# Kernel tuning notes

Hardware: AMD Instinct MI355X
Metric: run time of the kernel (lower is better)

Reference implementation:

```python
import jax, jax.numpy as jnp
import numpy as np
from jax import lax

B, C, H, W = 32, 256, 56, 56
NH, LC, DIL = 8, 7, 8  # heads, window size, dilation; H == LC*DIL -> exact dilated partition
N = LC * LC
DH = C // NH
SCALE = DH ** (-0.5)


def _rel_index():
    ch = np.arange(LC)
    coords = np.stack(np.meshgrid(ch, ch, indexing='ij')).reshape(2, -1)  # (2, 49)
    rel = (coords[:, :, None] - coords[:, None, :]).transpose(1, 2, 0)  # (49,49,2)
    rel[..., 0] += LC - 1
    rel[..., 1] += LC - 1
    rel[..., 0] *= 2 * LC - 1
    return jnp.asarray(rel.sum(-1))  # (49,49) int

REL_IDX = _rel_index()


def _layernorm(x, w, b, eps=1e-5):
    m = x.mean(-1, keepdims=True)
    v = ((x - m) ** 2).mean(-1, keepdims=True)
    return (x - m) * lax.rsqrt(v + eps) * w + b


def setup_inputs() -> dict:
    key = jax.random.key(0)
    ks = jax.random.split(key, 8)
    def n(k, shape, s=0.02):
        return jax.random.normal(k, shape, jnp.float32) * s
    return {
        'x': jax.random.normal(ks[0], (B, C, H, W), jnp.float32),
        'cpe_w': n(ks[1], (C, 1, 3, 3)),
        'cpe_b': jnp.zeros((C,), jnp.float32),
        'ln1_w': jnp.ones((C,), jnp.float32),
        'ln1_b': jnp.zeros((C,), jnp.float32),
        'rpb': n(ks[2], ((2 * LC - 1) ** 2, NH)),
        'qkv_w': n(ks[3], (C, 3 * C)),
        'qkv_b': jnp.zeros((3 * C,), jnp.float32),
        'proj_w': n(ks[4], (C, C)),
        'proj_b': jnp.zeros((C,), jnp.float32),
        'ln2_w': jnp.ones((C,), jnp.float32),
        'ln2_b': jnp.zeros((C,), jnp.float32),
        'fc1_w': n(ks[5], (C, 4 * C)),
        'fc1_b': jnp.zeros((4 * C,), jnp.float32),
        'fc2_w': n(ks[6], (4 * C, C)),
        'fc2_b': jnp.zeros((C,), jnp.float32),
    }


def reference(x, cpe_w, cpe_b, ln1_w, ln1_b, rpb, qkv_w, qkv_b, proj_w, proj_b,
              ln2_w, ln2_b, fc1_w, fc1_b, fc2_w, fc2_b):
    # CPE: depthwise 3x3 conv, residual
    cpe = lax.conv_general_dilated(x, cpe_w, (1, 1), 'SAME',
                                   dimension_numbers=('NCHW', 'OIHW', 'NCHW'),
                                   feature_group_count=C)
    x = x + cpe + cpe_b[None, :, None, None]
    x = x.transpose(0, 2, 3, 1)  # B,H,W,C
    shortcut = x
    xn = _layernorm(x, ln1_w, ln1_b)
    # dilated window partition (LD!=0): window (i,j) gathers pixels (i+DIL*t, j+DIL*u)
    xw = xn.reshape(B, LC, DIL, LC, DIL, C).transpose(0, 2, 4, 1, 3, 5)  # B,i,j,t,u,C
    x1 = xw.reshape(B * DIL * DIL, N, C)
    # window attention with relative position bias
    qkv = (x1 @ qkv_w + qkv_b).reshape(-1, N, 3, NH, DH).transpose(2, 0, 3, 1, 4)
    q, k, v = qkv[0] * SCALE, qkv[1], qkv[2]  # (Bn,NH,N,DH)
    attn = jnp.einsum('bhnd,bhmd->bhnm', q, k)
    bias = rpb[REL_IDX].transpose(2, 0, 1)  # (NH,N,N)
    attn = jax.nn.softmax(attn + bias[None], axis=-1)
    o = jnp.einsum('bhnm,bhmd->bhnd', attn, v).transpose(0, 2, 1, 3).reshape(-1, N, C)
    o = o @ proj_w + proj_b
    # scatter windows back to spatial positions (exact inverse of the partition)
    o = o.reshape(B, DIL, DIL, LC, LC, C).transpose(0, 3, 1, 4, 2, 5).reshape(B, H, W, C)
    x = shortcut + o
    h = _layernorm(x, ln2_w, ln2_b)
    h = jax.nn.gelu(h @ fc1_w + fc1_b, approximate=False) @ fc2_w + fc2_b
    x = x + h
    return x.transpose(0, 3, 1, 2)  # B,C,H,W
```

## Files before the change

kernel.cpp:

```cpp
#include <hip/hip_runtime.h>
#include <hip/hip_bf16.h>

#define DEVINL __device__ __forceinline__

constexpr int Cc  = 256;
constexpr int Hh  = 56;
constexpr int Ww  = 56;
constexpr int Tn  = 32 * 56 * 56;
constexpr int HW  = Hh * Ww;
constexpr float SCALEF = 0.17677669529663689f;

typedef __attribute__((ext_vector_type(4))) float f32x4;
typedef __attribute__((ext_vector_type(8))) short bf16x8;

DEVINL unsigned short f2bf(float f) {
  __hip_bfloat16 h = __float2bfloat16(f);
  return *reinterpret_cast<unsigned short*>(&h);
}
DEVINL float bf2f(unsigned short u) {
  union { unsigned int i; float f; } v; v.i = (unsigned int)u << 16; return v.f;
}
DEVINL float gelu_fast(float v) {
  const float z = 1.5957691f * (v + 0.044715f * v * v * v);
  return v / (1.0f + __expf(-z));
}

#define GLOAD_LDS16(gp, lp) \
  __builtin_amdgcn_global_load_lds((const __attribute__((address_space(1))) void*)(gp), \
                                   (__attribute__((address_space(3))) void*)(lp), 16, 0, 0)

__global__ __launch_bounds__(256) void cpe_kernel(const float* __restrict__ x,
    const float* __restrict__ cw, const float* __restrict__ cb,
    unsigned short* __restrict__ out)
{
  __shared__ unsigned short Xs[16 * 620];
  const int tid = threadIdx.x;
  const int bx  = blockIdx.x;
  const int cg  = bx & 15;
  const int t2  = bx >> 4;
  const int hg  = t2 % 7;
  const int b   = t2 / 7;
  const int c0  = cg * 16;
  const int h0  = hg * 8;

  for (int idx = tid; idx < 16 * 580; idx += 256) {
    const int ci  = idx / 580;
    const int rem = idx - ci * 580;
    const int rr  = rem / 58;
    const int wc  = rem - rr * 58;
    const int h2  = h0 - 1 + rr;
    const int w2  = wc - 1;
    float v = 0.f;
    if (h2 >= 0 && h2 < Hh && w2 >= 0 && w2 < Ww)
      v = x[((size_t)(b * Cc + c0 + ci)) * HW + h2 * Ww + w2];
    Xs[ci * 620 + rr * 60 + wc] = f2bf(v);
  }
  __syncthreads();

  const int ci = tid & 15;
  const int c  = c0 + ci;
  float wr9[9];
  #pragma unroll
  for (int i = 0; i < 9; ++i) wr9[i] = cw[c * 9 + i];
  const float cbv = cb[c];
  const unsigned short* Xc = Xs + ci * 620;

  #pragma unroll
  for (int it = 0; it < 7; ++it) {
    const int tg   = it * 16 + (tid >> 4);
    const int tok0 = tg * 4;
    const int hr   = tok0 / 56;
    const int w0   = tok0 - hr * 56;
    float rv[3][6];
    #pragma unroll
    for (int j = 0; j < 3; ++j) {
      const ushort4 a = *reinterpret_cast<const ushort4*>(Xc + (hr + j) * 60 + w0);
      const ushort2 e = *reinterpret_cast<const ushort2*>(Xc + (hr + j) * 60 + w0 + 4);
      rv[j][0] = bf2f(a.x); rv[j][1] = bf2f(a.y); rv[j][2] = bf2f(a.z);
      rv[j][3] = bf2f(a.w); rv[j][4] = bf2f(e.x); rv[j][5] = bf2f(e.y);
    }
    unsigned short ov[4];
    #pragma unroll
    for (int t = 0; t < 4; ++t) {
      float acc = rv[1][t + 1];
      acc += wr9[0] * rv[0][t] + wr9[1] * rv[0][t + 1] + wr9[2] * rv[0][t + 2];
      acc += wr9[3] * rv[1][t] + wr9[4] * rv[1][t + 1] + wr9[5] * rv[1][t + 2];
      acc += wr9[6] * rv[2][t] + wr9[7] * rv[2][t + 1] + wr9[8] * rv[2][t + 2];
      ov[t] = f2bf(acc + cbv);
    }
    const size_t tbase = (size_t)b * HW + (h0 + hr) * Ww + w0;
    #pragma unroll
    for (int t = 0; t < 4; ++t)
      out[(tbase + t) * Cc + c] = ov[t];
  }
}

__global__ __launch_bounds__(256) void stats_bf16(const unsigned short* __restrict__ in,
    float2* __restrict__ st)
{
  const int lane = threadIdx.x & 63;
  const size_t t = (size_t)blockIdx.x * 4 + (threadIdx.x >> 6);
  const ushort4 v = *reinterpret_cast<const ushort4*>(in + t * Cc + lane * 4);
  const float v0 = bf2f(v.x), v1 = bf2f(v.y), v2 = bf2f(v.z), v3 = bf2f(v.w);
  float s  = v0 + v1 + v2 + v3;
  float sq = v0 * v0 + v1 * v1 + v2 * v2 + v3 * v3;
  #pragma unroll
  for (int o = 32; o >= 1; o >>= 1) {
    s  += __shfl_xor(s, o);
    sq += __shfl_xor(sq, o);
  }
  if (lane == 0) {
    const float mean = s * (1.0f / Cc);
    const float var  = sq * (1.0f / Cc) - mean * mean;
    st[t] = make_float2(mean, rsqrtf(var + 1e-5f));
  }
}

template<int QS>
__global__ __launch_bounds__(256) void wconv_kernel(const float* __restrict__ W,
    const float* __restrict__ g, unsigned short* __restrict__ Wt, int K, int N)
{
  __shared__ float Xs[32][33];
  const int kb = blockIdx.x * 32, nb = blockIdx.y * 32;
  const int tn = threadIdx.x & 31, tk = threadIdx.x >> 5;
  #pragma unroll
  for (int i = 0; i < 4; ++i) {
    const int k = kb + tk + i * 8;
    const float gv = g ? g[k] : 1.0f;
    Xs[tk + i * 8][tn] = W[(size_t)k * N + nb + tn] * gv;
  }
  __syncthreads();
  const int wk = threadIdx.x & 31, wn = threadIdx.x >> 5;
  #pragma unroll
  for (int i = 0; i < 4; ++i) {
    const int n = nb + wn + i * 8;
    const float s = (QS && n < 256) ? SCALEF : 1.0f;
    Wt[(size_t)n * K + kb + wk] = f2bf(Xs[wk][wn + i * 8] * s);
  }
}

template<int S>
__global__ __launch_bounds__(256) void colsum_kernel(const float* __restrict__ W,
    const float* __restrict__ g, const float* __restrict__ bvec,
    const float* __restrict__ bias, float* __restrict__ C1, float* __restrict__ CB,
    int K, int N)
{
  __shared__ float red[2][256];
  const int col = blockIdx.x * 64 + (threadIdx.x & 63);
  const int ks  = threadIdx.x >> 6;
  const int kq  = K >> 2;
  float a1 = 0.f, a2 = 0.f;
  for (int k = ks * kq; k < (ks + 1) * kq; ++k) {
    const float wv = W[(size_t)k * N + col];
    a1 += g[k] * wv;
    a2 += bvec[k] * wv;
  }
  red[0][threadIdx.x] = a1;
  red[1][threadIdx.x] = a2;
  __syncthreads();
  if (threadIdx.x < 64) {
    float s1 = 0.f, s2 = 0.f;
    #pragma unroll
    for (int i = 0; i < 4; ++i) { s1 += red[0][threadIdx.x + i * 64]; s2 += red[1][threadIdx.x + i * 64]; }
    const float sc = (S && col < 256) ? SCALEF : 1.0f;
    C1[col] = sc * s1;
    CB[col] = sc * (s2 + bias[col]);
  }
}

__global__ __launch_bounds__(256) void biasgen_kernel(const float* __restrict__ rpb,
    float* __restrict__ biasT)
{
  const int i = blockIdx.x * 256 + threadIdx.x;
  const int h = i >> 12, n = (i >> 6) & 63, m = i & 63;
  float v;
  if (m >= 49) {
    v = -1e30f;
  } else {
    const int nc = n < 49 ? n : 48;
    const int dI = nc / 7 - m / 7 + 6;
    const int dJ = nc % 7 - m % 7 + 6;
    v = rpb[(dI * 13 + dJ) * 8 + h];
  }
  biasT[i] = v;
}

template<int EPI, int OSW>
__global__ __launch_bounds__(256) void mfma_gemm(
    const unsigned short* __restrict__ A, const unsigned short* __restrict__ Bt,
    const float* __restrict__ bias, const float* __restrict__ C1,
    const float2* __restrict__ stats, const unsigned short* __restrict__ resp,
    void* __restrict__ outp, int K, int N, int row0, int n_outer, int n_inner)
{
  __shared__ unsigned short Asm[128 * 64];
  __shared__ unsigned short Bsm[128 * 64];
  const int tid  = threadIdx.x;
  const int lane = tid & 63;
  const int wid  = tid >> 6;
  const int wr   = wid >> 1;
  const int wc   = wid & 1;

  const int slot  = blockIdx.x >> 3;
  const int outer = (slot / n_inner) * 8 + (blockIdx.x & 7);
  const int inner = slot - (slot / n_inner) * n_inner;
  if (outer >= n_outer) return;
  const int bm = (OSW ? inner : outer) * 128;
  const int bn = (OSW ? outer : inner) * 128;

  f32x4 acc[4][4] = {};

  const int srow = (lane >> 3);
  const int skc  = ((lane & 7) ^ srow) * 8;

  for (int k0 = 0; k0 < K; k0 += 64) {
    #pragma unroll
    for (int i = 0; i < 4; ++i) {
      const int ch  = wid * 4 + i;
      const int row = ch * 8 + srow;
      GLOAD_LDS16(A  + (size_t)(bm + row) * K + k0 + skc, &Asm[ch * 512]);
      GLOAD_LDS16(Bt + (size_t)(bn + row) * K + k0 + skc, &Bsm[ch * 512]);
    }
    __syncthreads();

    const int xr = lane & 7;
    const int lg = lane >> 4;
    #pragma unroll
    for (int k32 = 0; k32 < 2; ++k32) {
      const int koff = ((k32 * 4 + lg) ^ xr) * 8;
      bf16x8 af[4], bv[4];
      #pragma unroll
      for (int f = 0; f < 4; ++f) {
        af[f] = *reinterpret_cast<const bf16x8*>(
            &Asm[(wr * 64 + f * 16 + (lane & 15)) * 64 + koff]);
        bv[f] = *reinterpret_cast<const bf16x8*>(
            &Bsm[(wc * 64 + f * 16 + (lane & 15)) * 64 + koff]);
      }
      #pragma unroll
      for (int fm = 0; fm < 4; ++fm)
        #pragma unroll
        for (int fn = 0; fn < 4; ++fn)
          acc[fm][fn] = __builtin_amdgcn_mfma_f32_16x16x32_bf16(
              af[fm], bv[fn], acc[fm][fn], 0, 0, 0);
    }
    __syncthreads();
  }

  const int lr4 = (lane >> 4) * 4;
  const int lc  = lane & 15;
  if constexpr (EPI == 0 || EPI == 5) {
    float rsv[4][4], rmv[4][4];
    #pragma unroll
    for (int fm = 0; fm < 4; ++fm)
      #pragma unroll
      for (int r = 0; r < 4; ++r) {
        const float2 st = stats[bm + wr * 64 + fm * 16 + lr4 + r];
        rsv[fm][r] = st.y;
        rmv[fm][r] = -st.y * st.x;
      }
    #pragma unroll
    for (int fn = 0; fn < 4; ++fn) {
      const int gcol = bn + wc * 64 + fn * 16 + lc;
      const float c1 = C1[gcol], cb = bias[gcol];
      #pragma unroll
      for (int fm = 0; fm < 4; ++fm)
        #pragma unroll
        for (int r = 0; r < 4; ++r) {
          const int grow = bm + wr * 64 + fm * 16 + lr4 + r;
          float v = rsv[fm][r] * acc[fm][fn][r] + rmv[fm][r] * c1 + cb;
          if constexpr (EPI == 5) v = gelu_fast(v);
          ((unsigned short*)outp)[(size_t)grow * N + gcol] = f2bf(v);
        }
    }
  } else if constexpr (EPI == 4) {
    float bch[4][4];
    #pragma unroll
    for (int fm = 0; fm < 4; ++fm)
      #pragma unroll
      for (int r = 0; r < 4; ++r)
        bch[fm][r] = bias[bm + wr * 64 + fm * 16 + lr4 + r];
    #pragma unroll
    for (int fn = 0; fn < 4; ++fn) {
      const int gtok = bn + wc * 64 + fn * 16 + lc;
      const int mg = row0 + gtok;
      const int b  = mg / HW;
      const int sp = mg - b * HW;
      float* ob = (float*)outp + (size_t)b * 256 * HW + sp;
      #pragma unroll
      for (int fm = 0; fm < 4; ++fm)
        #pragma unroll
        for (int r = 0; r < 4; ++r) {
          const int ch = bm + wr * 64 + fm * 16 + lr4 + r;
          float v = acc[fm][fn][r] + bch[fm][r];
          v += bf2f(resp[(size_t)gtok * 256 + ch]);
          ob[(size_t)ch * HW] = v;
        }
    }
  } else {
    #pragma unroll
    for (int fn = 0; fn < 4; ++fn) {
      const int gcol = bn + wc * 64 + fn * 16 + lc;
      const float bvs = bias[gcol];
      #pragma unroll
      for (int fm = 0; fm < 4; ++fm) {
        #pragma unroll
        for (int r = 0; r < 4; ++r) {
          const int grow = bm + wr * 64 + fm * 16 + lr4 + r;
          float v = acc[fm][fn][r] + bvs;
          v += bf2f(resp[(size_t)grow * 256 + gcol]);
          ((unsigned short*)outp)[(size_t)grow * N + gcol] = f2bf(v);
        }
      }
    }
  }
}

__global__ __launch_bounds__(256) void attn_mfma(const unsigned short* __restrict__ qkv,
    const float* __restrict__ biasT, unsigned short* __restrict__ outD)
{
  __shared__ char smem[4 * 14848];
  const int tid  = threadIdx.x;
  const int lane = tid & 63;
  const int wid  = tid >> 6;
  char* base = smem + wid * 14848;
  char* Qs = base;
  char* Ks = base + 5120;
  char* Vt = base + 10240;
  char* Ps = base;

  const int blk = blockIdx.x;
  const int b   = blk >> 6;
  const int di  = (blk >> 3) & 7;
  const int dj  = blk & 7;
  const size_t t00 = (size_t)b * HW + di * Ww + dj;

  const int lg = lane >> 4;
  const int lc = lane & 15;

  for (int rep = 0; rep < 2; ++rep) {
    const int h = wid * 2 + rep;

    for (int i = lane; i < 300; i += 64) {
      if (i < 150) reinterpret_cast<unsigned long long*>(Qs + 49 * 80)[i] = 0ull;
      else         reinterpret_cast<unsigned long long*>(Ks + 49 * 80)[i - 150] = 0ull;
    }
    for (int i = lane; i < 192; i += 64) {
      const int row = i / 6, q = i - (i / 6) * 6;
      *reinterpret_cast<unsigned long long*>(Vt + row * 144 + 96 + q * 8) = 0ull;
    }

    for (int idx = lane; idx < 392; idx += 64) {
      const int row = idx >> 3, dq = idx & 7;
      const int li = row / 7, lj = row - (row / 7) * 7;
      const size_t t = t00 + (size_t)(li * 8) * Ww + lj * 8;
      const unsigned short* src = qkv + t * 768 + h * 32 + dq * 4;
      *reinterpret_cast<uint2*>(Qs + row * 80 + dq * 8) =
          *reinterpret_cast<const uint2*>(src);
      *reinterpret_cast<uint2*>(Ks + row * 80 + dq * 8) =
          *reinterpret_cast<const uint2*>(src + 256);
    }
    for (int idx = lane; idx < 784; idx += 64) {
      const int row = idx >> 4, q = idx & 15;
      const int li = row / 7, lj = row - (row / 7) * 7;
      const size_t t = t00 + (size_t)(li * 8) * Ww + lj * 8;
      const unsigned int v = *reinterpret_cast<const unsigned int*>(
          qkv + t * 768 + h * 32 + 512 + q * 2);
      *reinterpret_cast<unsigned short*>(Vt + (2 * q) * 144 + row * 2) =
          (unsigned short)(v & 0xffff);
      *reinterpret_cast<unsigned short*>(Vt + (2 * q + 1) * 144 + row * 2) =
          (unsigned short)(v >> 16);
    }

    f32x4 sacc[4][4] = {};
    {
      bf16x8 af[4], bv[4];
      #pragma unroll
      for (int f = 0; f < 4; ++f) {
        af[f] = *reinterpret_cast<const bf16x8*>(Qs + (f * 16 + lc) * 80 + lg * 16);
        bv[f] = *reinterpret_cast<const bf16x8*>(Ks + (f * 16 + lc) * 80 + lg * 16);
      }
      #pragma unroll
      for (int fm = 0; fm < 4; ++fm)
        #pragma unroll
        for (int fn = 0; fn < 4; ++fn)
          sacc[fm][fn] = __builtin_amdgcn_mfma_f32_16x16x32_bf16(
              af[fm], bv[fn], sacc[fm][fn], 0, 0, 0);
    }

    const float* bh = biasT + h * 4096;
    #pragma unroll
    for (int fm = 0; fm < 4; ++fm) {
      float rowv[4][4];
      #pragma unroll
      for (int r = 0; r < 4; ++r) {
        const int n = fm * 16 + lg * 4 + r;
        #pragma unroll
        for (int fn = 0; fn < 4; ++fn)
          rowv[r][fn] = sacc[fm][fn][r] + bh[n * 64 + fn * 16 + lc];
      }
      #pragma unroll
      for (int r = 0; r < 4; ++r) {
        float mx = fmaxf(fmaxf(rowv[r][0], rowv[r][1]), fmaxf(rowv[r][2], rowv[r][3]));
        #pragma unroll
        for (int o = 8; o >= 1; o >>= 1) mx = fmaxf(mx, __shfl_xor(mx, o));
        float p[4], sm = 0.f;
        #pragma unroll
        for (int fn = 0; fn < 4; ++fn) { p[fn] = __expf(rowv[r][fn] - mx); sm += p[fn]; }
        #pragma unroll
        for (int o = 8; o >= 1; o >>= 1) sm += __shfl_xor(sm, o);
        const float inv = 1.0f / sm;
        const int n = fm * 16 + lg * 4 + r;
        #pragma unroll
        for (int fn = 0; fn < 4; ++fn)
          *reinterpret_cast<unsigned short*>(Ps + n * 144 + (fn * 16 + lc) * 2) =
              f2bf(p[fn] * inv);
      }
    }

    f32x4 oacc[4][2] = {};
    #pragma unroll
    for (int ks = 0; ks < 2; ++ks) {
      bf16x8 pa[4], vb[2];
      #pragma unroll
      for (int fm = 0; fm < 4; ++fm)
        pa[fm] = *reinterpret_cast<const bf16x8*>(
            Ps + (fm * 16 + lc) * 144 + ks * 64 + lg * 16);
      #pragma unroll
      for (int fn = 0; fn < 2; ++fn)
        vb[fn] = *reinterpret_cast<const bf16x8*>(
            Vt + (fn * 16 + lc) * 144 + ks * 64 + lg * 16);
      #pragma unroll
      for (int fm = 0; fm < 4; ++fm)
        #pragma unroll
        for (int fn = 0; fn < 2; ++fn)
          oacc[fm][fn] = __builtin_amdgcn_mfma_f32_16x16x32_bf16(
              pa[fm], vb[fn], oacc[fm][fn], 0, 0, 0);
    }

    #pragma unroll
    for (int fm = 0; fm < 4; ++fm) {
      #pragma unroll
      for (int r = 0; r < 4; ++r) {
        const int n = fm * 16 + lg * 4 + r;
        if (n < 49) {
          const int li = n / 7, lj = n - (n / 7) * 7;
          const size_t t = t00 + (size_t)(li * 8) * Ww + lj * 8;
          outD[t * 256 + h * 32 + lc]      = f2bf(oacc[fm][0][r]);
          outD[t * 256 + h * 32 + 16 + lc] = f2bf(oacc[fm][1][r]);
        }
      }
    }
  }
}

extern "C" void kernel_launch(void* const* d_in, const int* in_sizes, int n_in,
                              void* d_out, int out_size, void* d_ws, size_t ws_size,
                              hipStream_t stream) {
  (void)in_sizes; (void)n_in; (void)out_size;
  const float* x      = (const float*)d_in[0];
  const float* cpe_w  = (const float*)d_in[1];
  const float* cpe_b  = (const float*)d_in[2];
  const float* ln1_w  = (const float*)d_in[3];
  const float* ln1_b  = (const float*)d_in[4];
  const float* rpb    = (const float*)d_in[5];
  const float* qkv_w  = (const float*)d_in[6];
  const float* qkv_b  = (const float*)d_in[7];
  const float* proj_w = (const float*)d_in[8];
  const float* proj_b = (const float*)d_in[9];
  const float* ln2_w  = (const float*)d_in[10];
  const float* ln2_b  = (const float*)d_in[11];
  const float* fc1_w  = (const float*)d_in[12];
  const float* fc1_b  = (const float*)d_in[13];
  const float* fc2_w  = (const float*)d_in[14];
  const float* fc2_b  = (const float*)d_in[15];

  char* ws = (char*)d_ws;
  unsigned short* qkv_wt  = (unsigned short*)(ws);
  unsigned short* proj_wt = (unsigned short*)(ws + 393216);
  unsigned short* fc1_wt  = (unsigned short*)(ws + 524288);
  unsigned short* fc2_wt  = (unsigned short*)(ws + 1048576);
  float*  C1q = (float*)(ws + 1572864);
  float*  CBq = (float*)(ws + 1575936);
  float*  C1f = (float*)(ws + 1579008);
  float*  CBf = (float*)(ws + 1583104);

  const int NB_rt = (ws_size >= 311000000ull) ? 32 : 8;
  const int MCHrt = NB_rt * HW;
  const int NCH   = 32 / NB_rt;
  const int NOUT  = MCHrt / 128;
  const int NOUTP = (NOUT + 7) & ~7;

  unsigned short *slotX, *slotQ, *slotE;
  float2* stats1Full = nullptr;
  float*  biasTp;
  if (NB_rt == 8) {
    slotX  = (unsigned short*)(ws + 1587200);
    slotQ  = (unsigned short*)(ws + 1587200 + 12845056);
    slotE  = (unsigned short*)(ws + 1587200 + 12845056 + 51380224);
    biasTp = (float*)((char*)slotE + 200704);
  } else {
    biasTp     = (float*)(ws + 1587200);
    stats1Full = (float2*)(ws + 1718272);
    size_t o = 2521088;
    slotX = (unsigned short*)(ws + o); o += (size_t)MCHrt * 256 * 2;
    slotQ = (unsigned short*)(ws + o); o += (size_t)MCHrt * 1024 * 2;
    slotE = (unsigned short*)(ws + o);
  }

  unsigned short* Araw = (unsigned short*)d_out + 25690112;

  wconv_kernel<1><<<dim3(8, 24), 256, 0, stream>>>(qkv_w,  ln1_w,  qkv_wt,  256, 768);
  wconv_kernel<0><<<dim3(8, 8),  256, 0, stream>>>(proj_w, nullptr, proj_wt, 256, 256);
  wconv_kernel<0><<<dim3(8, 32), 256, 0, stream>>>(fc1_w,  ln2_w,  fc1_wt,  256, 1024);
  wconv_kernel<0><<<dim3(32, 8), 256, 0, stream>>>(fc2_w,  nullptr, fc2_wt,  1024, 256);
  colsum_kernel<1><<<12, 256, 0, stream>>>(qkv_w, ln1_w, ln1_b, qkv_b, C1q, CBq, 256, 768);
  colsum_kernel<0><<<16, 256, 0, stream>>>(fc1_w, ln2_w, ln2_b, fc1_b, C1f, CBf, 256, 1024);

  cpe_kernel<<<32 * 7 * 16, 256, 0, stream>>>(x, cpe_w, cpe_b, Araw);

  if (NB_rt != 8) {
    stats_bf16<<<Tn / 4, 256, 0, stream>>>(Araw, stats1Full);
    biasgen_kernel<<<128, 256, 0, stream>>>(rpb, biasTp);
  }

  for (int c = 0; c < NCH; ++c) {
    const int r0 = c * MCHrt;
    const unsigned short* Ac = Araw + (size_t)r0 * Cc;
    const float2* stp1;
    if (NB_rt == 8) {
      float2* stloc = (float2*)slotE;
      stats_bf16<<<MCHrt / 4, 256, 0, stream>>>(Ac, stloc);
      biasgen_kernel<<<128, 256, 0, stream>>>(rpb, biasTp);
      stp1 = stloc;
    } else {
      stp1 = stats1Full + r0;
    }
    mfma_gemm<0, 0><<<NOUTP * 6, 256, 0, stream>>>(
        Ac, qkv_wt, CBq, C1q, stp1, nullptr, slotQ, 256, 768, 0, NOUT, 6);
    attn_mfma<<<NB_rt * 64, 256, 0, stream>>>(slotQ, biasTp, slotX);
    mfma_gemm<1, 0><<<NOUTP * 2, 256, 0, stream>>>(
        slotX, proj_wt, proj_b, nullptr, nullptr, Ac, slotE, 256, 256, 0, NOUT, 2);
    float2* stats2 = (float2*)slotX;
    stats_bf16<<<MCHrt / 4, 256, 0, stream>>>(slotE, stats2);
    mfma_gemm<5, 0><<<NOUTP * 8, 256, 0, stream>>>(
        slotE, fc1_wt, CBf, C1f, stats2, nullptr, slotQ, 256, 1024, 0, NOUT, 8);
    mfma_gemm<4, 1><<<NOUTP * 2, 256, 0, stream>>>(
        fc2_wt, slotQ, fc2_b, nullptr, nullptr, slotE, d_out, 1024, 256, r0, NOUT, 2);
  }
}
```

Measured before the change: 673.1 us.

## Fuse proj GEMM with residual add and LayerNorm stats; coalesce CPE loads

Adds a proj_fused kernel in which each block computes a full 128x256 output tile, adds the bias and residual, writes E, and reduces per-row sum and sum-of-squares into LN2 stats. This removes the separate stats_bf16 pass over E on the large-workspace path. The CPE kernel is also restructured so each 16-thread group loads contiguous row segments without per-element div/mod, and output token indexing is simplified. Risks: the full-width tile means fewer blocks and more accumulator registers, which can lower occupancy, and the stats use single-pass E[x^2]-mu^2.

```diff
diff --git a/kernel.cpp b/kernel.cpp
--- a/kernel.cpp
+++ b/kernel.cpp
@@ -43,17 +43,26 @@
   const int c0  = cg * 16;
   const int h0  = hg * 8;
 
-  for (int idx = tid; idx < 16 * 580; idx += 256) {
-    const int ci  = idx / 580;
-    const int rem = idx - ci * 580;
-    const int rr  = rem / 58;
-    const int wc  = rem - rr * 58;
-    const int h2  = h0 - 1 + rr;
-    const int w2  = wc - 1;
-    float v = 0.f;
-    if (h2 >= 0 && h2 < Hh && w2 >= 0 && w2 < Ww)
-      v = x[((size_t)(b * Cc + c0 + ci)) * HW + h2 * Ww + w2];
-    Xs[ci * 620 + rr * 60 + wc] = f2bf(v);
+  {
+    const int ci_s = tid >> 4;
+    const int sub  = tid & 15;
+    const float* xc = x + ((size_t)(b * Cc + c0 + ci_s)) * HW;
+    unsigned short* dch = Xs + ci_s * 620;
+    for (int r = 0; r < 10; ++r) {
+      const int h2 = h0 - 1 + r;
+      unsigned short* dst = dch + r * 60;
+      #pragma unroll
+      for (int p = 0; p < 4; ++p) {
+        const int wc = sub + p * 16;
+        if (wc < 58) {
+          const int w2 = wc - 1;
+          float v = 0.f;
+          if (h2 >= 0 && h2 < Hh && w2 >= 0 && w2 < Ww)
+            v = xc[h2 * Ww + w2];
+          dst[wc] = f2bf(v);
+        }
+      }
+    }
   }
   __syncthreads();
 
@@ -65,12 +74,14 @@
   const float cbv = cb[c];
   const unsigned short* Xc = Xs + ci * 620;
 
+  const int ty   = tid >> 4;
+  const int hr   = ty >> 1;
+  const int half = ty & 1;
+  const size_t tbase0 = (size_t)b * HW + (h0 + hr) * Ww;
+
   #pragma unroll
   for (int it = 0; it < 7; ++it) {
-    const int tg   = it * 16 + (tid >> 4);
-    const int tok0 = tg * 4;
-    const int hr   = tok0 / 56;
-    const int w0   = tok0 - hr * 56;
+    const int w0 = (half * 7 + it) * 4;
     float rv[3][6];
     #pragma unroll
     for (int j = 0; j < 3; ++j) {
@@ -88,10 +99,9 @@
       acc += wr9[6] * rv[2][t] + wr9[7] * rv[2][t + 1] + wr9[8] * rv[2][t + 2];
       ov[t] = f2bf(acc + cbv);
     }
-    const size_t tbase = (size_t)b * HW + (h0 + hr) * Ww + w0;
     #pragma unroll
     for (int t = 0; t < 4; ++t)
-      out[(tbase + t) * Cc + c] = ov[t];
+      out[(tbase0 + w0 + t) * Cc + c] = ov[t];
   }
 }
 
@@ -311,6 +321,107 @@
         }
       }
     }
+  }
+}
+
+__global__ __launch_bounds__(256) void proj_fused(
+    const unsigned short* __restrict__ A, const unsigned short* __restrict__ Bt,
+    const float* __restrict__ bias, const unsigned short* __restrict__ res,
+    unsigned short* __restrict__ Eout, float2* __restrict__ stats)
+{
+  __shared__ unsigned short Asm[128 * 64];
+  __shared__ unsigned short Bsm[256 * 64];
+  const int tid  = threadIdx.x;
+  const int lane = tid & 63;
+  const int wid  = tid >> 6;
+  const int wr   = wid >> 1;
+  const int wc   = wid & 1;
+  const int bm   = blockIdx.x * 128;
+
+  f32x4 acc[4][8] = {};
+
+  const int srow = lane >> 3;
+  const int skc  = ((lane & 7) ^ srow) * 8;
+
+  for (int k0 = 0; k0 < 256; k0 += 64) {
+    #pragma unroll
+    for (int i = 0; i < 12; ++i) {
+      const int ch = wid * 12 + i;
+      if (ch < 16) {
+        const int row = ch * 8 + srow;
+        GLOAD_LDS16(A + (size_t)(bm + row) * 256 + k0 + skc, &Asm[ch * 512]);
+      } else {
+        const int row = (ch - 16) * 8 + srow;
+        GLOAD_LDS16(Bt + (size_t)row * 256 + k0 + skc, &Bsm[(ch - 16) * 512]);
+      }
+    }
+    __syncthreads();
+
+    const int xr = lane & 7;
+    const int lg = lane >> 4;
+    #pragma unroll
+    for (int k32 = 0; k32 < 2; ++k32) {
+      const int koff = ((k32 * 4 + lg) ^ xr) * 8;
+      bf16x8 af[4], bv[8];
+      #pragma unroll
+      for (int f = 0; f < 4; ++f)
+        af[f] = *reinterpret_cast<const bf16x8*>(
+            &Asm[(wr * 64 + f * 16 + (lane & 15)) * 64 + koff]);
+      #pragma unroll
+      for (int f = 0; f < 8; ++f)
+        bv[f] = *reinterpret_cast<const bf16x8*>(
+            &Bsm[(wc * 128 + f * 16 + (lane & 15)) * 64 + koff]);
+      #pragma unroll
+      for (int fm = 0; fm < 4; ++fm)
+        #pragma unroll
+        for (int fn = 0; fn < 8; ++fn)
+          acc[fm][fn] = __builtin_amdgcn_mfma_f32_16x16x32_bf16(
+              af[fm], bv[fn], acc[fm][fn], 0, 0, 0);
+    }
+    __syncthreads();
+  }
+
+  const int lr4 = (lane >> 4) * 4;
+  const int lc  = lane & 15;
+  float pbv[8];
+  #pragma unroll
+  for (int fn = 0; fn < 8; ++fn) pbv[fn] = bias[wc * 128 + fn * 16 + lc];
+
+  float* sred = reinterpret_cast<float*>(Asm);
+  #pragma unroll
+  for (int fm = 0; fm < 4; ++fm) {
+    #pragma unroll
+    for (int r = 0; r < 4; ++r) {
+      const int rho  = wr * 64 + fm * 16 + lr4 + r;
+      const int grow = bm + rho;
+      float s1 = 0.f, s2 = 0.f;
+      #pragma unroll
+      for (int fn = 0; fn < 8; ++fn) {
+        const int gcol = wc * 128 + fn * 16 + lc;
+        float e = acc[fm][fn][r] + pbv[fn];
+        e += bf2f(res[(size_t)grow * 256 + gcol]);
+        Eout[(size_t)grow * 256 + gcol] = f2bf(e);
+        s1 += e;
+        s2 += e * e;
+      }
+      #pragma unroll
+      for (int o = 8; o >= 1; o >>= 1) {
+        s1 += __shfl_xor(s1, o);
+        s2 += __shfl_xor(s2, o);
+      }
+      if (lc == 0) {
+        sred[rho * 4 + wc * 2 + 0] = s1;
+        sred[rho * 4 + wc * 2 + 1] = s2;
+      }
+    }
+  }
+  __syncthreads();
+  if (tid < 128) {
+    const float S  = sred[tid * 4 + 0] + sred[tid * 4 + 2];
+    const float SQ = sred[tid * 4 + 1] + sred[tid * 4 + 3];
+    const float mu = S * (1.0f / 256.0f);
+    const float var = SQ * (1.0f / 256.0f) - mu * mu;
+    stats[bm + tid] = make_float2(mu, rsqrtf(var + 1e-5f));
   }
 }
 
@@ -490,7 +601,7 @@
   const int NOUTP = (NOUT + 7) & ~7;
 
   unsigned short *slotX, *slotQ, *slotE;
-  float2* stats1Full = nullptr;
+  float2* statsFull = nullptr;
   float*  biasTp;
   if (NB_rt == 8) {
     slotX  = (unsigned short*)(ws + 1587200);
@@ -498,8 +609,8 @@
     slotE  = (unsigned short*)(ws + 1587200 + 12845056 + 51380224);
     biasTp = (float*)((char*)slotE + 200704);
   } else {
-    biasTp     = (float*)(ws + 1587200);
-    stats1Full = (float2*)(ws + 1718272);
+    biasTp    = (float*)(ws + 1587200);
+    statsFull = (float2*)(ws + 1718272);
     size_t o = 2521088;
     slotX = (unsigned short*)(ws + o); o += (size_t)MCHrt * 256 * 2;
     slotQ = (unsigned short*)(ws + o); o += (size_t)MCHrt * 1024 * 2;
@@ -518,32 +629,39 @@
   cpe_kernel<<<32 * 7 * 16, 256, 0, stream>>>(x, cpe_w, cpe_b, Araw);
 
   if (NB_rt != 8) {
-    stats_bf16<<<Tn / 4, 256, 0, stream>>>(Araw, stats1Full);
+    stats_bf16<<<Tn / 4, 256, 0, stream>>>(Araw, statsFull);
     biasgen_kernel<<<128, 256, 0, stream>>>(rpb, biasTp);
   }
 
   for (int c = 0; c < NCH; ++c) {
     const int r0 = c * MCHrt;
     const unsigned short* Ac = Araw + (size_t)r0 * Cc;
-    const float2* stp1;
+
     if (NB_rt == 8) {
       float2* stloc = (float2*)slotE;
       stats_bf16<<<MCHrt / 4, 256, 0, stream>>>(Ac, stloc);
       biasgen_kernel<<<128, 256, 0, stream>>>(rpb, biasTp);
-      stp1 = stloc;
+      mfma_gemm<0, 0><<<NOUTP * 6, 256, 0, stream>>>(
+          Ac, qkv_wt, CBq, C1q, stloc, nullptr, slotQ, 256, 768, 0, NOUT, 6);
+      attn_mfma<<<NB_rt * 64, 256, 0, stream>>>(slotQ, biasTp, slotX);
+      mfma_gemm<1, 0><<<NOUTP * 2, 256, 0, stream>>>(
+          slotX, proj_wt, proj_b, nullptr, nullptr, Ac, slotE, 256, 256, 0, NOUT, 2);
+      float2* stats2 = (float2*)slotX;
+      stats_bf16<<<MCHrt / 4, 256, 0, stream>>>(slotE, stats2);
+      mfma_gemm<5, 0><<<NOUTP * 8, 256, 0, stream>>>(
+          slotE, fc1_wt, CBf, C1f, stats2, nullptr, slotQ, 256, 1024, 0, NOUT, 8);
+      mfma_gemm<4, 1><<<NOUTP * 2, 256, 0, stream>>>(
+          fc2_wt, slotQ, fc2_b, nullptr, nullptr, slotE, d_out, 1024, 256, r0, NOUT, 2);
     } else {
-      stp1 = stats1Full + r0;
-    }
-    mfma_gemm<0, 0><<<NOUTP * 6, 256, 0, stream>>>(
-        Ac, qkv_wt, CBq, C1q, stp1, nullptr, slotQ, 256, 768, 0, NOUT, 6);
-    attn_mfma<<<NB_rt * 64, 256, 0, stream>>>(slotQ, biasTp, slotX);
-    mfma_gemm<1, 0><<<NOUTP * 2, 256, 0, stream>>>(
-        slotX, proj_wt, proj_b, nullptr, nullptr, Ac, slotE, 256, 256, 0, NOUT, 2);
-    float2* stats2 = (float2*)slotX;
-    stats_bf16<<<MCHrt / 4, 256, 0, stream>>>(slotE, stats2);
-    mfma_gemm<5, 0><<<NOUTP * 8, 256, 0, stream>>>(
-        slotE, fc1_wt, CBf, C1f, stats2, nullptr, slotQ, 256, 1024, 0, NOUT, 8);
-    mfma_gemm<4, 1><<<NOUTP * 2, 256, 0, stream>>>(
-        fc2_wt, slotQ, fc2_b, nullptr, nullptr, slotE, d_out, 1024, 256, r0, NOUT, 2);
-  }
-}
+      mfma_gemm<0, 0><<<NOUTP * 6, 256, 0, stream>>>(
+          Ac, qkv_wt, CBq, C1q, statsFull, nullptr, slotQ, 256, 768, 0, NOUT, 6);
+      attn_mfma<<<NB_rt * 64, 256, 0, stream>>>(slotQ, biasTp, slotX);
+      proj_fused<<<NOUT, 256, 0, stream>>>(
+          slotX, proj_wt, proj_b, Ac, slotE, statsFull);
+      mfma_gemm<5, 0><<<NOUTP * 8, 256, 0, stream>>>(
+          slotE, fc1_wt, CBf, C1f, statsFull, nullptr, slotQ, 256, 1024, 0, NOUT, 8);
+      mfma_gemm<4, 1><<<NOUTP * 2, 256, 0, stream>>>(
+          fc2_wt, slotQ, fc2_b, nullptr, nullptr, slotE, d_out, 1024, 256, r0, NOUT, 2);
+    }
+  }
+}
```

Result: slower. 707.0 us (+5.0%).
